# Optimization experiments

Measured on AMD Instinct MI355X. Metric: run time of the kernel, lower is better.

The kernel has to match this reference:

```python
import jax, jax.numpy as jnp
import numpy as np

NUM_VECTORS = 1024
LATENT_DIM = 256
BETA = 0.25


def setup_inputs() -> dict:
    key = jax.random.key(0)
    k1, k2 = jax.random.split(key)
    x = jax.random.normal(k1, (32, LATENT_DIM, 64, 64), dtype=jnp.float32)
    # torch init: uniform(-1/num_vectors, 1/num_vectors)
    emb = jax.random.uniform(k2, (NUM_VECTORS, LATENT_DIM), dtype=jnp.float32,
                             minval=-1.0 / NUM_VECTORS, maxval=1.0 / NUM_VECTORS)
    return {"x": x, "emb": emb}


def reference(x, emb):
    B, C, H, W = x.shape
    x_bhwc = jnp.transpose(x, (0, 2, 3, 1))          # [B,H,W,C]
    xf = x_bhwc.reshape(-1, C)                       # [N,C], N = B*H*W
    d = (jnp.sum(xf * xf, axis=1, keepdims=True)
         + jnp.sum(emb * emb, axis=1)
         - 2.0 * (xf @ emb.T))
    idx = jnp.argmin(d, axis=1)                      # [N]
    x_q = emb[idx].reshape(B, H, W, C)               # gather + reshape
    sg = jax.lax.stop_gradient
    loss = (jnp.mean((sg(x_q) - x_bhwc) ** 2)
            + BETA * jnp.mean((x_q - sg(x_bhwc)) ** 2))
    # straight-through estimator
    x_q_st = x_bhwc + sg(x_q - x_bhwc)
    x_q_out = jnp.transpose(x_q_st, (0, 3, 1, 2))    # [B,C,H,W]
    return (x_q_out, idx, loss)
```

## Files before the change

kernel.cpp:

```cpp
#include <hip/hip_runtime.h>
#include <cfloat>

#define NV    1024
#define CDIM  256
#define NROWS 131072
#define TOTAL 33554432
#define HW    4096
#define WWIN  3.5e-4f
#define MST   68

typedef __attribute__((ext_vector_type(8))) short bf16x8;
typedef __attribute__((ext_vector_type(4))) float f32x4;

template <typename GET>
__device__ __forceinline__ float np_s128(const GET& get, int base) {
    float tv[16];
#pragma unroll
    for (int l = 0; l < 16; ++l) {
        float s0 = __fadd_rn(get(base + l),      get(base + 64 + l));
        float s1 = __fadd_rn(get(base + 16 + l), get(base + 80 + l));
        float s2 = __fadd_rn(get(base + 32 + l), get(base + 96 + l));
        float s3 = __fadd_rn(get(base + 48 + l), get(base + 112 + l));
        tv[l] = __fadd_rn(__fadd_rn(s0, s1), __fadd_rn(s2, s3));
    }
    float u[8];
#pragma unroll
    for (int l = 0; l < 8; ++l) u[l] = __fadd_rn(tv[l], tv[l + 8]);
    float v[4];
#pragma unroll
    for (int l = 0; l < 4; ++l) v[l] = __fadd_rn(u[l], u[l + 4]);
    return __fadd_rn(__fadd_rn(v[0], v[2]), __fadd_rn(v[1], v[3]));
}
template <typename GET>
__device__ __forceinline__ float np_s256(const GET& get) {
    return __fadd_rn(np_s128(get, 0), np_s128(get, 128));
}

__device__ __forceinline__ unsigned short f2bf_rne(float f) {
    unsigned u = __float_as_uint(f);
    unsigned r = u + 0x7fffu + ((u >> 16) & 1u);
    return (unsigned short)(r >> 16);
}

__device__ __forceinline__ float exact_d(const float* __restrict__ xrow,
                                         const float* __restrict__ erow,
                                         float sxn, float se) {
    float g = 0.f;
    for (int c = 0; c < CDIM; ++c) g = __fmaf_rn(xrow[c], erow[c], g);
    return __fsub_rn(__fadd_rn(sxn, se), __fmul_rn(2.0f, g));
}

__device__ __forceinline__ void gload_lds16(const void* gsrc, void* ldst) {
    __builtin_amdgcn_global_load_lds(
        (const __attribute__((address_space(1))) void*)gsrc,
        (__attribute__((address_space(3))) void*)ldst, 16, 0, 0);
}

__global__ void zero_hdr(double* loss, int* fbcnt) {
    if (threadIdx.x == 0) { *loss = 0.0; *fbcnt = 0; }
}

__global__ void enorm_kernel(const float* __restrict__ emb, float* __restrict__ enf) {
    int k = blockIdx.x * blockDim.x + threadIdx.x;
    if (k < NV) {
        const float* e = emb + (size_t)k * CDIM;
        auto get = [e](int c) { return __fmul_rn(e[c], e[c]); };
        enf[k] = np_s256(get);
    }
}

__global__ void esplit_kernel(const float* __restrict__ emb,
                              unsigned short* __restrict__ ehg) {
    int i = blockIdx.x * blockDim.x + threadIdx.x;
    if (i < NV * CDIM) ehg[i] = f2bf_rne(emb[i]);
}

__global__ __launch_bounds__(256, 2) void gemm_argmin_kernel(
        const float* __restrict__ x, const float* __restrict__ emb,
        const unsigned short* __restrict__ ehg,
        const float* __restrict__ enf, int* __restrict__ idx,
        int* __restrict__ fb_list, int* __restrict__ fb_cnt) {
    __shared__ __align__(16) char sbuf[32768];
    __shared__ __align__(16) float senf[NV];

    const int tid  = threadIdx.x;
    const int lane = tid & 63;
    const int lcol = lane & 15;
    const int quad = lane >> 4;
    const int wid  = tid >> 6;
    const int wy   = wid >> 1;
    const int wx   = wid & 1;
    const int mbase = wy * 32;
    const int nl   = wx * 16 + lcol;

    const int rowbase = blockIdx.x * 64;
    const int b   = rowbase >> 12;
    const int hw0 = rowbase & 4095;
    const float* xb = x + ((size_t)b * CDIM) * HW + hw0;

    auto STAGE = [&](int buf, int ch) {
        char* dB = sbuf + (buf << 14);
        const int k0 = ch * 32;
#pragma unroll
        for (int it = 0; it < 4; ++it) {
            const int g  = it * 256 + tid;
            const int n  = g >> 5, p = g & 31;
            const int s5 = (p - n) & 31;
            const size_t src = (size_t)(k0 + n) * 256 + s5 * 8;
            gload_lds16(ehg + src, dB + g * 16);
        }
    };

    STAGE(0, 0);

    *(float4*)&senf[tid * 4] = *(const float4*)&enf[tid * 4];

    bf16x8 ah[2][8];
#pragma unroll
    for (int t = 0; t < 2; ++t) {
        const int m = mbase + t * 16 + lcol;
#pragma unroll
        for (int kc = 0; kc < 8; ++kc) {
            const int c0 = kc * 32 + quad * 8;
            float fv[8];
#pragma unroll
            for (int j = 0; j < 8; ++j) fv[j] = xb[(size_t)(c0 + j) * HW + m];
#pragma unroll
            for (int j = 0; j < 8; ++j) ah[t][kc][j] = (short)f2bf_rne(fv[j]);
        }
    }

    float m1[8], m2[8];
#pragma unroll
    for (int s = 0; s < 8; ++s) { m1[s] = FLT_MAX; m2[s] = FLT_MAX; }
    unsigned i1p[2] = { 0xffffffffu, 0xffffffffu };

    __syncthreads();

    int cur = 0;
    for (int ch = 0; ch < 32; ++ch) {
        if (ch < 31) STAGE(cur ^ 1, ch + 1);

        const unsigned short* sBh = (const unsigned short*)(sbuf + (cur << 14));
        const int k0 = ch * 32;

        const float enfv = senf[k0 + nl];
        f32x4 acc[2];
        acc[0] = (f32x4){0.f, 0.f, 0.f, 0.f};
        acc[1] = (f32x4){0.f, 0.f, 0.f, 0.f};

#pragma unroll
        for (int kc = 0; kc < 8; ++kc) {
            const int s5  = kc * 4 + quad;
            const int off = nl * 256 + (((s5 + nl) & 31) * 8);
            const bf16x8 bh = *(const bf16x8*)&sBh[off];
#pragma unroll
            for (int t = 0; t < 2; ++t)
                acc[t] = __builtin_amdgcn_mfma_f32_16x16x32_bf16(
                    ah[t][kc], bh, acc[t], 0, 0, 0);
        }

#pragma unroll
        for (int t = 0; t < 2; ++t)
#pragma unroll
            for (int r = 0; r < 4; ++r) {
                const float z = __fmaf_rn(-2.0f, acc[t][r], enfv);
                const int s  = t * 4 + r;
                const int sh = r * 8;
                const bool lt1 = z < m1[s];
                m2[s] = __builtin_amdgcn_fmed3f(z, m1[s], m2[s]);
                m1[s] = fminf(z, m1[s]);
                const unsigned cand = (i1p[t] & ~(0xffu << sh)) | ((unsigned)ch << sh);
                i1p[t] = lt1 ? cand : i1p[t];
            }

        __syncthreads();
        cur ^= 1;
    }

    float* Mv1 = (float*)sbuf;
    int*   Mi1 = (int*)(sbuf + 8704);
    float* Mv2 = (float*)(sbuf + 17408);
#pragma unroll
    for (int t = 0; t < 2; ++t) {
        const int row0 = mbase + t * 16 + quad * 4;
        const int base = nl * MST + row0;
        *(float4*)&Mv1[base] = *(const float4*)&m1[t * 4];
        *(float4*)&Mv2[base] = *(const float4*)&m2[t * 4];
        int4 kk;
        kk.x = (int)((i1p[t] >>  0) & 0xffu) * 32 + nl;
        kk.y = (int)((i1p[t] >>  8) & 0xffu) * 32 + nl;
        kk.z = (int)((i1p[t] >> 16) & 0xffu) * 32 + nl;
        kk.w = (int)((i1p[t] >> 24) & 0xffu) * 32 + nl;
        *(int4*)&Mi1[base] = kk;
    }
    __syncthreads();

    if (tid < 64) {
        const int row = tid;
        float M = FLT_MAX;
#pragma unroll
        for (int c = 0; c < 32; ++c) M = fminf(M, Mv1[c * MST + row]);
        const float lim = M + WWIN;

        int cand[12]; int cnt = 0; bool overflow = false;
        for (int c = 0; c < 32; ++c) {
            if (Mv2[c * MST + row] <= lim) overflow = true;
            if (Mv1[c * MST + row] <= lim) {
                if (cnt < 12) cand[cnt++] = Mi1[c * MST + row] & (NV - 1);
                else overflow = true;
            }
        }
        if (overflow) {
            const int pos = atomicAdd(fb_cnt, 1);
            fb_list[pos] = rowbase + row;
        } else if (cnt == 1) {
            idx[rowbase + row] = cand[0];
        } else {
            auto g2 = [xb, row](int c) {
                const float v = xb[(size_t)c * HW + row];
                return __fmul_rn(v, v);
            };
            const float sxn = np_s256(g2);
            float bd = FLT_MAX; int bk = 0x7fffffff;
            for (int cc = 0; cc < cnt; ++cc) {
                const int kk = cand[cc];
                const float* er = emb + (size_t)kk * CDIM;
                float gacc = 0.f;
                for (int c2 = 0; c2 < CDIM; ++c2)
                    gacc = __fmaf_rn(xb[(size_t)c2 * HW + row], er[c2], gacc);
                const float d = __fsub_rn(__fadd_rn(sxn, senf[kk]),
                                          __fmul_rn(2.0f, gacc));
                if (d < bd || (d == bd && kk < bk)) { bd = d; bk = kk; }
            }
            idx[rowbase + row] = bk;
        }
    }
}

__global__ __launch_bounds__(256) void fallback_kernel(
        const float* __restrict__ x, const float* __restrict__ emb,
        const float* __restrict__ enf, int* __restrict__ idx,
        const int* __restrict__ fb_list, const int* __restrict__ fb_cnt) {
    __shared__ float sxr[CDIM];
    __shared__ float rv[256];
    __shared__ int   rk[256];

    const int n = *fb_cnt;
    for (int i = blockIdx.x; i < n; i += gridDim.x) {
        const int r  = fb_list[i];
        const int b  = r >> 12;
        const int hw = r & 4095;
        sxr[threadIdx.x] = x[((size_t)(b * CDIM + threadIdx.x)) * HW + hw];
        __syncthreads();

        auto get = [](int c) { float v = ((const float*)sxr)[c]; return __fmul_rn(v, v); };
        float sxn = np_s256(get);

        float bd = FLT_MAX; int bk = 0x7fffffff;
#pragma unroll
        for (int j = 0; j < 4; ++j) {
            const int k = threadIdx.x * 4 + j;
            float d = exact_d(sxr, emb + (size_t)k * CDIM, sxn, enf[k]);
            if (d < bd) { bd = d; bk = k; }
        }
        rv[threadIdx.x] = bd; rk[threadIdx.x] = bk;
        __syncthreads();
        for (int sft = 128; sft > 0; sft >>= 1) {
            if (threadIdx.x < sft) {
                float ov = rv[threadIdx.x + sft]; int ok = rk[threadIdx.x + sft];
                if (ov < rv[threadIdx.x] ||
                    (ov == rv[threadIdx.x] && ok < rk[threadIdx.x])) {
                    rv[threadIdx.x] = ov; rk[threadIdx.x] = ok;
                }
            }
            __syncthreads();
        }
        if (threadIdx.x == 0) idx[r] = rk[0];
        __syncthreads();
    }
}

__global__ __launch_bounds__(256) void gather_kernel(
        const float* __restrict__ x, const float* __restrict__ emb,
        const int* __restrict__ idx, float* __restrict__ out,
        double* __restrict__ loss) {
    __shared__ float sE[64][260];
    __shared__ int   sidx[64];
    __shared__ double red[256];

    const int tid = threadIdx.x;
    const int rowbase = blockIdx.x * 64;
    const int b   = rowbase >> 12;
    const int hw0 = rowbase & 4095;

    if (tid < 64) sidx[tid] = idx[rowbase + tid];
    __syncthreads();

    {
        const int r  = tid >> 2;
        const int qt = tid & 3;
        const float* e = emb + (size_t)sidx[r] * CDIM + qt * 64;
        for (int u = 0; u < 16; ++u) {
            float4 v = *(const float4*)(e + u * 4);
            *(float4*)&sE[r][qt * 64 + u * 4] = v;
        }
    }
    __syncthreads();

    const float* xb = x + ((size_t)b * CDIM) * HW + hw0;
    float* ob = out + ((size_t)b * CDIM) * HW + hw0;
    double s = 0.0;
    for (int it = 0; it < 16; ++it) {
        int c  = it * 16 + (tid >> 4);
        int m4 = (tid & 15) * 4;
        float4 ev;
        ev.x = sE[m4 + 0][c]; ev.y = sE[m4 + 1][c];
        ev.z = sE[m4 + 2][c]; ev.w = sE[m4 + 3][c];
        float4 xv = *(const float4*)(xb + (size_t)c * HW + m4);
        *(float4*)(ob + (size_t)c * HW + m4) = ev;
        float d0 = ev.x - xv.x, d1 = ev.y - xv.y, d2 = ev.z - xv.z, d3 = ev.w - xv.w;
        s = fma((double)d0, (double)d0, s);
        s = fma((double)d1, (double)d1, s);
        s = fma((double)d2, (double)d2, s);
        s = fma((double)d3, (double)d3, s);
    }
    red[tid] = s;
    __syncthreads();
    for (int sft = 128; sft > 0; sft >>= 1) {
        if (tid < sft) red[tid] += red[tid + sft];
        __syncthreads();
    }
    if (tid == 0) atomicAdd(loss, red[0]);
}

__global__ void idxout_kernel(const int* __restrict__ idx, float* __restrict__ oidx) {
    int r = blockIdx.x * blockDim.x + threadIdx.x;
    if (r < NROWS) oidx[r] = (float)idx[r];
}

__global__ void fin_kernel(const double* __restrict__ loss, float* __restrict__ o) {
    *o = (float)(1.25 * (*loss) / (double)TOTAL);
}

extern "C" void kernel_launch(void* const* d_in, const int* in_sizes, int n_in,
                              void* d_out, int out_size, void* d_ws, size_t ws_size,
                              hipStream_t stream) {
    const float* x   = (const float*)d_in[0];
    const float* emb = (const float*)d_in[1];
    float* out = (float*)d_out;
    char*  ws  = (char*)d_ws;

    double* loss    = (double*)ws;
    int*    fb_cnt  = (int*)(ws + 8);
    float*  enf     = (float*)(ws + 64);
    int*    idx     = (int*)(ws + 64 + 4096);
    int*    fb_list = idx + NROWS;

    unsigned short* ehg = (unsigned short*)d_out;

    float* out_xq   = out;
    float* out_idx  = out + (size_t)TOTAL;
    float* out_loss = out + (size_t)TOTAL + NROWS;

    hipLaunchKernelGGL(zero_hdr,         dim3(1),            dim3(64),  0, stream, loss, fb_cnt);
    hipLaunchKernelGGL(enorm_kernel,     dim3(4),            dim3(256), 0, stream, emb, enf);
    hipLaunchKernelGGL(esplit_kernel,    dim3(NV * CDIM / 256), dim3(256), 0, stream, emb, ehg);
    hipLaunchKernelGGL(gemm_argmin_kernel, dim3(NROWS / 64), dim3(256), 0, stream,
                       x, emb, ehg, enf, idx, fb_list, fb_cnt);
    hipLaunchKernelGGL(fallback_kernel,  dim3(256),          dim3(256), 0, stream,
                       x, emb, enf, idx, fb_list, fb_cnt);
    hipLaunchKernelGGL(gather_kernel,    dim3(NROWS / 64),   dim3(256), 0, stream,
                       x, emb, idx, out_xq, loss);
    hipLaunchKernelGGL(idxout_kernel,    dim3(NROWS / 256),  dim3(256), 0, stream, idx, out_idx);
    hipLaunchKernelGGL(fin_kernel,       dim3(1),            dim3(1),   0, stream, loss, out_loss);
}
```

Baseline: 487.5 us.

## Load codebook B fragments directly from global memory and fuse index output into gather

The GEMM-argmin kernel stops staging bf16 codebook tiles into double-buffered LDS with global_load_lds and per-chunk barriers, and instead reads each B fragment directly from global memory (L2-resident, 512 KB). This shrinks LDS use to the epilogue's needs and removes the per-chunk __syncthreads. Separately, the index-to-float output is written inside gather_kernel, so idxout_kernel and its launch go away. The cost is that global load latency is no longer hidden by an explicit prefetch, and each wave re-fetches B data that was previously shared through LDS.

```diff
diff --git a/kernel.cpp b/kernel.cpp
--- a/kernel.cpp
+++ b/kernel.cpp
@@ -50,12 +50,6 @@
     return __fsub_rn(__fadd_rn(sxn, se), __fmul_rn(2.0f, g));
 }
 
-__device__ __forceinline__ void gload_lds16(const void* gsrc, void* ldst) {
-    __builtin_amdgcn_global_load_lds(
-        (const __attribute__((address_space(1))) void*)gsrc,
-        (__attribute__((address_space(3))) void*)ldst, 16, 0, 0);
-}
-
 __global__ void zero_hdr(double* loss, int* fbcnt) {
     if (threadIdx.x == 0) { *loss = 0.0; *fbcnt = 0; }
 }
@@ -80,7 +74,7 @@
         const unsigned short* __restrict__ ehg,
         const float* __restrict__ enf, int* __restrict__ idx,
         int* __restrict__ fb_list, int* __restrict__ fb_cnt) {
-    __shared__ __align__(16) char sbuf[32768];
+    __shared__ __align__(16) char sbuf[26112];
     __shared__ __align__(16) float senf[NV];
 
     const int tid  = threadIdx.x;
@@ -98,21 +92,6 @@
     const int hw0 = rowbase & 4095;
     const float* xb = x + ((size_t)b * CDIM) * HW + hw0;
 
-    auto STAGE = [&](int buf, int ch) {
-        char* dB = sbuf + (buf << 14);
-        const int k0 = ch * 32;
-#pragma unroll
-        for (int it = 0; it < 4; ++it) {
-            const int g  = it * 256 + tid;
-            const int n  = g >> 5, p = g & 31;
-            const int s5 = (p - n) & 31;
-            const size_t src = (size_t)(k0 + n) * 256 + s5 * 8;
-            gload_lds16(ehg + src, dB + g * 16);
-        }
-    };
-
-    STAGE(0, 0);
-
     *(float4*)&senf[tid * 4] = *(const float4*)&enf[tid * 4];
 
     bf16x8 ah[2][8];
@@ -137,28 +116,24 @@
 
     __syncthreads();
 
-    int cur = 0;
+    const unsigned short* bp = ehg + (size_t)nl * 256 + quad * 8;
+
+#pragma unroll 1
     for (int ch = 0; ch < 32; ++ch) {
-        if (ch < 31) STAGE(cur ^ 1, ch + 1);
-
-        const unsigned short* sBh = (const unsigned short*)(sbuf + (cur << 14));
-        const int k0 = ch * 32;
-
-        const float enfv = senf[k0 + nl];
+        const float enfv = senf[ch * 32 + nl];
         f32x4 acc[2];
         acc[0] = (f32x4){0.f, 0.f, 0.f, 0.f};
         acc[1] = (f32x4){0.f, 0.f, 0.f, 0.f};
 
 #pragma unroll
         for (int kc = 0; kc < 8; ++kc) {
-            const int s5  = kc * 4 + quad;
-            const int off = nl * 256 + (((s5 + nl) & 31) * 8);
-            const bf16x8 bh = *(const bf16x8*)&sBh[off];
-#pragma unroll
-            for (int t = 0; t < 2; ++t)
-                acc[t] = __builtin_amdgcn_mfma_f32_16x16x32_bf16(
-                    ah[t][kc], bh, acc[t], 0, 0, 0);
-        }
+            const bf16x8 bh = *(const bf16x8*)(bp + kc * 32);
+            acc[0] = __builtin_amdgcn_mfma_f32_16x16x32_bf16(
+                ah[0][kc], bh, acc[0], 0, 0, 0);
+            acc[1] = __builtin_amdgcn_mfma_f32_16x16x32_bf16(
+                ah[1][kc], bh, acc[1], 0, 0, 0);
+        }
+        bp += 32 * 256;
 
 #pragma unroll
         for (int t = 0; t < 2; ++t)
@@ -173,9 +148,6 @@
                 const unsigned cand = (i1p[t] & ~(0xffu << sh)) | ((unsigned)ch << sh);
                 i1p[t] = lt1 ? cand : i1p[t];
             }
-
-        __syncthreads();
-        cur ^= 1;
     }
 
     float* Mv1 = (float*)sbuf;
@@ -284,7 +256,7 @@
 __global__ __launch_bounds__(256) void gather_kernel(
         const float* __restrict__ x, const float* __restrict__ emb,
         const int* __restrict__ idx, float* __restrict__ out,
-        double* __restrict__ loss) {
+        float* __restrict__ oidx, double* __restrict__ loss) {
     __shared__ float sE[64][260];
     __shared__ int   sidx[64];
     __shared__ double red[256];
@@ -296,6 +268,8 @@
 
     if (tid < 64) sidx[tid] = idx[rowbase + tid];
     __syncthreads();
+
+    if (tid < 64) oidx[rowbase + tid] = (float)sidx[tid];
 
     {
         const int r  = tid >> 2;
@@ -334,11 +308,6 @@
     if (tid == 0) atomicAdd(loss, red[0]);
 }
 
-__global__ void idxout_kernel(const int* __restrict__ idx, float* __restrict__ oidx) {
-    int r = blockIdx.x * blockDim.x + threadIdx.x;
-    if (r < NROWS) oidx[r] = (float)idx[r];
-}
-
 __global__ void fin_kernel(const double* __restrict__ loss, float* __restrict__ o) {
     *o = (float)(1.25 * (*loss) / (double)TOTAL);
 }
@@ -371,7 +340,6 @@
     hipLaunchKernelGGL(fallback_kernel,  dim3(256),          dim3(256), 0, stream,
                        x, emb, enf, idx, fb_list, fb_cnt);
     hipLaunchKernelGGL(gather_kernel,    dim3(NROWS / 64),   dim3(256), 0, stream,
-                       x, emb, idx, out_xq, loss);
-    hipLaunchKernelGGL(idxout_kernel,    dim3(NROWS / 256),  dim3(256), 0, stream, idx, out_idx);
+                       x, emb, idx, out_xq, out_idx, loss);
     hipLaunchKernelGGL(fin_kernel,       dim3(1),            dim3(1),   0, stream, loss, out_loss);
 }
```

After: 603.3 us. +23.8%, slower.
